# Kernel optimization log

Hardware: AMD Instinct MI355X
Metric: run time of the kernel (lower is better)

Reference implementation:

```python
import jax, jax.numpy as jnp
import numpy as np

B, S, D, H = 2, 2048, 1024, 16
HEAD_DIM = D // H
SCALE = HEAD_DIM ** -0.5


def setup_inputs() -> dict:
    key = jax.random.key(0)
    k1, k2, k3 = jax.random.split(key, 3)
    x = jax.random.normal(k1, (B, S, D), dtype=jnp.float32)
    # torch nn.Linear convention: weight is [out_features, in_features], y = x @ W.T + b
    W_qkv = jax.random.normal(k2, (3 * D, D), dtype=jnp.float32) * 0.02  # qkv Linear, bias=False
    W_out = jax.random.normal(k3, (D, D), dtype=jnp.float32) * 0.02
    b_out = jnp.zeros((D,), dtype=jnp.float32)
    return {"x": x, "W_qkv": W_qkv, "W_out": W_out, "b_out": b_out}


def reference(x, W_qkv, W_out, b_out):
    b, s, d_model = x.shape
    # qkv projection (no bias), then split 'b c (qkv h d) -> qkv b h c d'
    qkv = (x @ W_qkv.T).reshape(b, s, 3, H, HEAD_DIM).transpose(2, 0, 3, 1, 4)
    q, k, v = qkv[0], qkv[1], qkv[2]  # each [b, h, s, hd]
    # naive full attention: scores materialized as [b, h, s, s]
    attn = jax.nn.softmax(jnp.einsum('bhxd,bhyd->bhxy', q, k) * SCALE, axis=-1)
    # dropout is identity (rate 0 / eval mode)
    o = jnp.einsum('bhxy,bhyd->bhxd', attn, v)
    o = o.transpose(0, 2, 1, 3).reshape(b, s, d_model)  # 'b h c d -> b c (h d)'
    return o @ W_out.T + b_out
```

## Files before the change

kernel.cpp:

```cpp
#include <hip/hip_runtime.h>


typedef __attribute__((ext_vector_type(8))) short short8;
typedef __attribute__((ext_vector_type(4))) float f32x4;
typedef unsigned short ushort_t;
typedef unsigned int uint32;

#define AS1 __attribute__((address_space(1)))
#define AS3 __attribute__((address_space(3)))

__device__ __forceinline__ void gload_lds16(const void* gp, void* lp) {
    __builtin_amdgcn_global_load_lds((const AS1 void*)gp, (AS3 void*)lp, 16, 0, 0);
}

#if __has_builtin(__builtin_amdgcn_exp2f)
#define EXP2F(x) __builtin_amdgcn_exp2f(x)
#else
#define EXP2F(x) exp2f(x)
#endif

__device__ __forceinline__ uint32 rhu(float f) { return __float_as_uint(f) + 0x8000u; }
#if __has_builtin(__builtin_amdgcn_perm)
__device__ __forceinline__ uint32 pk2bf(float a, float b) {
    return __builtin_amdgcn_perm(rhu(b), rhu(a), 0x07060302u);
}
#else
__device__ __forceinline__ uint32 pk2bf(float a, float b) {
    return (rhu(a) >> 16) | (rhu(b) & 0xffff0000u);
}
#endif
__device__ __forceinline__ ushort_t f2bf(float f) { return (ushort_t)(rhu(f) >> 16); }

__global__ void cvt_all(const float* __restrict__ x, ushort_t* __restrict__ xb,
                        const float* __restrict__ wq, ushort_t* __restrict__ wqb,
                        const float* __restrict__ wo, ushort_t* __restrict__ wob) {
    int blk = blockIdx.x;
    const float* in; ushort_t* out;
    if (blk < 4096)      { in = x;  out = xb;  }
    else if (blk < 7168) { in = wq; out = wqb; blk -= 4096; }
    else                 { in = wo; out = wob; blk -= 7168; }
    const int i = (blk * 256 + threadIdx.x) * 4;
    const float4 v = *(const float4*)(in + i);
    uint2 pk;
    pk.x = pk2bf(v.x, v.y);
    pk.y = pk2bf(v.z, v.w);
    *(uint2*)(out + i) = pk;
}

__global__ __launch_bounds__(256, 2)
void gemm_qkv(const ushort_t* __restrict__ A, const ushort_t* __restrict__ B,
              ushort_t* __restrict__ Cb, ushort_t* __restrict__ vT,
              int M, int N, int K, int ldc, float qScale) {
    __shared__ ushort_t lA[2][128 * 32];
    __shared__ ushort_t lB[2][128 * 32];
    const int tid = threadIdx.x;
    const int wave = tid >> 6, lane = tid & 63;
    const int quad = lane >> 4, l16 = lane & 15;
    const int wr = wave >> 1, wc = wave & 1;
    const int mBase = blockIdx.y * 128, nBase = blockIdx.x * 128;

    f32x4 acc[4][4];
#pragma unroll
    for (int i = 0; i < 4; i++)
#pragma unroll
        for (int j = 0; j < 4; j++) acc[i][j] = (f32x4){0.f, 0.f, 0.f, 0.f};

    const int ar = tid >> 2;
    const int ac = (((tid & 3) ^ ((ar >> 1) & 3)) * 8);
    const int rsw = ((l16 >> 1) & 3);

    const ushort_t* aptr = A + (size_t)(mBase + ar) * K + ac;
    const ushort_t* bptr = B + (size_t)(nBase + ar) * K + ac;

#define G1_STAGE(buf, k0)                                                            \
    {                                                                                \
        _Pragma("unroll") for (int c = 0; c < 2; c++) {                              \
            gload_lds16(aptr + (size_t)(c * 64) * K + (k0), lA[buf] + c * 2048 + wave * 512); \
            gload_lds16(bptr + (size_t)(c * 64) * K + (k0), lB[buf] + c * 2048 + wave * 512); \
        }                                                                            \
    }

    G1_STAGE(0, 0);
    for (int k0 = 0; k0 < K; k0 += 32) {
        const int cur = (k0 >> 5) & 1;
        __syncthreads();
        if (k0 + 32 < K) G1_STAGE(cur ^ 1, k0 + 32);

        short8 af[4], bf[4];
#pragma unroll
        for (int i = 0; i < 4; i++)
            af[i] = *(const short8*)(lA[cur] + (wr * 64 + i * 16 + l16) * 32 + ((quad ^ rsw) * 8));
#pragma unroll
        for (int j = 0; j < 4; j++)
            bf[j] = *(const short8*)(lB[cur] + (wc * 64 + j * 16 + l16) * 32 + ((quad ^ rsw) * 8));
#pragma unroll
        for (int i = 0; i < 4; i++)
#pragma unroll
            for (int j = 0; j < 4; j++)
                acc[i][j] = __builtin_amdgcn_mfma_f32_16x16x32_bf16(af[i], bf[j], acc[i][j], 0, 0, 0);
    }

    if (nBase >= 2048) {
#pragma unroll
        for (int i = 0; i < 4; i++)
#pragma unroll
            for (int j = 0; j < 4; j++) {
                const int row0 = mBase + wr * 64 + i * 16 + quad * 4;
                const int col = nBase + wc * 64 + j * 16 + l16 - 2048;
                const int b = row0 >> 11, s0 = row0 & 2047;
                uint2 pk;
                pk.x = pk2bf(acc[i][j][0], acc[i][j][1]);
                pk.y = pk2bf(acc[i][j][2], acc[i][j][3]);
                *(uint2*)(vT + ((size_t)(b * 16) * 64 + col) * 2048 + s0) = pk;
            }
        return;
    }
    const float cs = (nBase < 1024) ? qScale : 1.0f;
#pragma unroll
    for (int i = 0; i < 4; i++)
#pragma unroll
        for (int j = 0; j < 4; j++)
#pragma unroll
            for (int r = 0; r < 4; r++) {
                const int row = mBase + wr * 64 + i * 16 + quad * 4 + r;
                const int col = nBase + wc * 64 + j * 16 + l16;
                Cb[(size_t)row * ldc + col] = f2bf(acc[i][j][r] * cs);
            }
}

__global__ __launch_bounds__(256, 2)
void gemm_out(const ushort_t* __restrict__ A, const ushort_t* __restrict__ B,
              float* __restrict__ Cf, const float* __restrict__ bias,
              int M, int N, int K) {
    __shared__ ushort_t lA[2][64 * 64];
    __shared__ ushort_t lB[2][128 * 64];
    const int tid = threadIdx.x;
    const int wave = tid >> 6, lane = tid & 63;
    const int quad = lane >> 4, l16 = lane & 15;
    const int mBase = blockIdx.y * 64, nBase = blockIdx.x * 128;

    f32x4 acc[4][2];
#pragma unroll
    for (int i = 0; i < 4; i++)
#pragma unroll
        for (int j = 0; j < 2; j++) acc[i][j] = (f32x4){0.f, 0.f, 0.f, 0.f};

    const int sr = tid >> 3;
    const int sc = ((tid & 7) ^ (sr & 7)) * 8;
    const int swz = l16 & 7;

    const ushort_t* aptr = A + (size_t)(mBase + sr) * K + sc;
    const ushort_t* bptr = B + (size_t)(nBase + sr) * K + sc;

#define G2_STAGE(buf, k0)                                                              \
    {                                                                                  \
        _Pragma("unroll") for (int c = 0; c < 2; c++)                                  \
            gload_lds16(aptr + (size_t)(c * 32) * K + (k0), lA[buf] + c * 2048 + wave * 512); \
        _Pragma("unroll") for (int c = 0; c < 4; c++)                                  \
            gload_lds16(bptr + (size_t)(c * 32) * K + (k0), lB[buf] + c * 2048 + wave * 512); \
    }

    G2_STAGE(0, 0);
    for (int k0 = 0; k0 < K; k0 += 64) {
        const int cur = (k0 >> 6) & 1;
        __syncthreads();
        if (k0 + 64 < K) G2_STAGE(cur ^ 1, k0 + 64);

#pragma unroll
        for (int ks = 0; ks < 2; ks++) {
            short8 af[4], bf[2];
#pragma unroll
            for (int i = 0; i < 4; i++)
                af[i] = *(const short8*)(lA[cur] + (i * 16 + l16) * 64 + (((ks * 4 + quad) ^ swz) * 8));
#pragma unroll
            for (int j = 0; j < 2; j++)
                bf[j] = *(const short8*)(lB[cur] + (wave * 32 + j * 16 + l16) * 64 + (((ks * 4 + quad) ^ swz) * 8));
#pragma unroll
            for (int i = 0; i < 4; i++)
#pragma unroll
                for (int j = 0; j < 2; j++)
                    acc[i][j] = __builtin_amdgcn_mfma_f32_16x16x32_bf16(af[i], bf[j], acc[i][j], 0, 0, 0);
        }
    }

#pragma unroll
    for (int i = 0; i < 4; i++)
#pragma unroll
        for (int j = 0; j < 2; j++)
#pragma unroll
            for (int r = 0; r < 4; r++) {
                const int row = mBase + i * 16 + quad * 4 + r;
                const int col = nBase + wave * 32 + j * 16 + l16;
                Cf[(size_t)row * N + col] = acc[i][j][r] + bias[col];
            }
}

__global__ __launch_bounds__(512, 4)
void attn_flash(const ushort_t* __restrict__ qk, const ushort_t* __restrict__ vT,
                ushort_t* __restrict__ o) {
    __shared__ ushort_t smem[26624];

    const int tid = threadIdx.x;
    const int wave = tid >> 6, lane = tid & 63;
    const int quad = lane >> 4, l16 = lane & 15;
    const int qg = wave & 3, kg = wave >> 2;
    const int bh = blockIdx.y, b = bh >> 4, h = bh & 15;
    const size_t rowBase = (size_t)b * 2048;
    const int qCol = h * 64, kCol = 1024 + h * 64;
    const int qRow0 = blockIdx.x * 128;
    const int swz = l16 & 7;

    ushort_t* lP = smem + 16384 + wave * 1280;

    {
        const int sr_ = tid >> 3;
        const int sc_ = ((tid & 7) ^ (sr_ & 7)) * 8;
#pragma unroll
        for (int cc = 0; cc < 2; cc++)
            gload_lds16(qk + (rowBase + qRow0 + cc * 64 + sr_) * 2048 + qCol + sc_,
                        smem + 16384 + cc * 4096 + wave * 512);
    }
    __syncthreads();
    short8 qf[2][2];
#pragma unroll
    for (int qt = 0; qt < 2; qt++)
#pragma unroll
        for (int ks = 0; ks < 2; ks++)
            qf[qt][ks] = *(const short8*)(smem + 16384 + (qg * 32 + qt * 16 + l16) * 64 +
                                          (((ks * 4 + quad) ^ swz) * 8));
    __syncthreads();

    short8 onesA;
#pragma unroll
    for (int i = 0; i < 8; i++) onesA[i] = (short)0x3F80;

    f32x4 oacc[4][2];
    f32x4 lacc[2];
#pragma unroll
    for (int qt = 0; qt < 2; qt++) {
        lacc[qt] = (f32x4){0.f, 0.f, 0.f, 0.f};
#pragma unroll
        for (int dt = 0; dt < 4; dt++) oacc[dt][qt] = (f32x4){0.f, 0.f, 0.f, 0.f};
    }

    const int sr = tid >> 3;
    const int sch = ((tid & 7) ^ (sr & 7)) * 8;
    const ushort_t* kptr = qk + (rowBase + sr) * 2048 + kCol + sch;
    const ushort_t* vptr = vT + ((size_t)bh * 64 + sr) * 2048 + sch;

#define AT_STAGE(buf, kt)                                                            \
    {                                                                                \
        gload_lds16(kptr + (size_t)(kt) * 64 * 2048, smem + (buf) * 4096 + wave * 512); \
        gload_lds16(vptr + (kt) * 64, smem + 8192 + (buf) * 4096 + wave * 512);      \
    }

    AT_STAGE(0, 0);
    for (int kt = 0; kt < 32; kt++) {
        const int cur = kt & 1;
        __syncthreads();
        if (kt < 31) AT_STAGE(cur ^ 1, kt + 1);
        const ushort_t* lK = smem + cur * 4096;
        const ushort_t* lV = smem + 8192 + cur * 4096;

        f32x4 sacc[2][2];
#pragma unroll
        for (int mh = 0; mh < 2; mh++) {
            const int krow = kg * 32 + mh * 16 + l16;
            const short8 k0 = *(const short8*)(lK + krow * 64 + ((quad ^ swz) * 8));
            const short8 k1 = *(const short8*)(lK + krow * 64 + (((4 + quad) ^ swz) * 8));
#pragma unroll
            for (int qt = 0; qt < 2; qt++) {
                f32x4 t = (f32x4){0.f, 0.f, 0.f, 0.f};
                t = __builtin_amdgcn_mfma_f32_16x16x32_bf16(k0, qf[qt][0], t, 0, 0, 0);
                t = __builtin_amdgcn_mfma_f32_16x16x32_bf16(k1, qf[qt][1], t, 0, 0, 0);
                sacc[mh][qt] = t;
            }
        }

#pragma unroll
        for (int qt = 0; qt < 2; qt++)
#pragma unroll
            for (int mh = 0; mh < 2; mh++) {
                const f32x4 s = sacc[mh][qt];
                uint2 pk;
                pk.x = pk2bf(EXP2F(s[0]), EXP2F(s[1]));
                pk.y = pk2bf(EXP2F(s[2]), EXP2F(s[3]));
                *(uint2*)(&lP[(qt * 16 + l16) * 40 + mh * 16 + quad * 4]) = pk;
            }

        short8 pf[2];
#pragma unroll
        for (int qt = 0; qt < 2; qt++) {
            pf[qt] = *(const short8*)(&lP[(qt * 16 + l16) * 40 + quad * 8]);
            lacc[qt] = __builtin_amdgcn_mfma_f32_16x16x32_bf16(onesA, pf[qt], lacc[qt], 0, 0, 0);
        }
#pragma unroll
        for (int dt = 0; dt < 4; dt++) {
            const short8 vf = *(const short8*)(lV + (dt * 16 + l16) * 64 +
                                               (((kg * 4 + quad) ^ swz) * 8));
#pragma unroll
            for (int qt = 0; qt < 2; qt++)
                oacc[dt][qt] = __builtin_amdgcn_mfma_f32_16x16x32_bf16(vf, pf[qt], oacc[dt][qt], 0, 0, 0);
        }
    }

    __syncthreads();
    float* red = (float*)smem;
    if (kg == 1) {
#pragma unroll
        for (int qt = 0; qt < 2; qt++) {
            if (quad == 0) red[8192 + qg * 32 + qt * 16 + l16] = lacc[qt][0];
#pragma unroll
            for (int dt = 0; dt < 4; dt++)
                *(f32x4*)(red + (((qg * 4 + dt) * 2 + qt) * 64 + lane) * 4) = oacc[dt][qt];
        }
    }
    __syncthreads();
    if (kg == 0) {
        float linv[2];
#pragma unroll
        for (int qt = 0; qt < 2; qt++)
            linv[qt] = 1.0f / (lacc[qt][0] + red[8192 + qg * 32 + qt * 16 + l16]);
#pragma unroll
        for (int qt = 0; qt < 2; qt++) {
            const size_t row = rowBase + qRow0 + qg * 32 + qt * 16 + l16;
#pragma unroll
            for (int dt = 0; dt < 4; dt++) {
                const f32x4 r = *(const f32x4*)(red + (((qg * 4 + dt) * 2 + qt) * 64 + lane) * 4);
                uint2 pk;
                pk.x = pk2bf((oacc[dt][qt][0] + r[0]) * linv[qt],
                             (oacc[dt][qt][1] + r[1]) * linv[qt]);
                pk.y = pk2bf((oacc[dt][qt][2] + r[2]) * linv[qt],
                             (oacc[dt][qt][3] + r[3]) * linv[qt]);
                *(uint2*)(o + row * 1024 + h * 64 + dt * 16 + quad * 4) = pk;
            }
        }
    }
}

extern "C" void kernel_launch(void* const* d_in, const int* in_sizes, int n_in,
                              void* d_out, int out_size, void* d_ws, size_t ws_size,
                              hipStream_t stream) {
    const float* x    = (const float*)d_in[0];
    const float* Wqkv = (const float*)d_in[1];
    const float* Wout = (const float*)d_in[2];
    const float* bout = (const float*)d_in[3];
    float* out = (float*)d_out;

    ushort_t* xb    = (ushort_t*)d_ws;
    ushort_t* wqkvb = xb + (size_t)4096 * 1024;
    ushort_t* woutb = wqkvb + (size_t)3072 * 1024;
    ushort_t* qkb   = woutb + (size_t)1024 * 1024;
    ushort_t* vTb   = qkb + (size_t)4096 * 2048;
    ushort_t* ob    = xb;

    const float SC = 0.125f * 1.44269504089f;

    cvt_all<<<8192, 256, 0, stream>>>(x, xb, Wqkv, wqkvb, Wout, woutb);
    gemm_qkv<<<dim3(24, 32), 256, 0, stream>>>(xb, wqkvb, qkb, vTb, 4096, 3072, 1024, 2048, SC);
    attn_flash<<<dim3(16, 32), 512, 0, stream>>>(qkb, vTb, ob);
    gemm_out<<<dim3(8, 64), 256, 0, stream>>>(ob, woutb, out, bout, 4096, 1024, 1024);
}
```

Measured before the change: 181.4 us.

## Fuse fp32-to-bf16 conversion into GEMM loads, drop separate convert kernel

Removes the standalone cvt_all kernel. The QKV and output-projection GEMMs now read fp32 inputs and weights directly into registers, pack them to bf16, and write them to shared memory after the MFMA loop, in place of asynchronous global-to-LDS loads. This avoids a kernel launch and a full round trip of bf16 copies through global memory. In exchange the GEMMs read twice the bytes, hold more registers for the staging buffers, and the qkv GEMM's launch bound rises to 3 blocks per CU.

Measured after the change: 186.0 us. 1.03x slower.

```diff
diff --git a/kernel.cpp b/kernel.cpp
--- a/kernel.cpp
+++ b/kernel.cpp
@@ -31,24 +31,15 @@
 #endif
 __device__ __forceinline__ ushort_t f2bf(float f) { return (ushort_t)(rhu(f) >> 16); }
 
-__global__ void cvt_all(const float* __restrict__ x, ushort_t* __restrict__ xb,
-                        const float* __restrict__ wq, ushort_t* __restrict__ wqb,
-                        const float* __restrict__ wo, ushort_t* __restrict__ wob) {
-    int blk = blockIdx.x;
-    const float* in; ushort_t* out;
-    if (blk < 4096)      { in = x;  out = xb;  }
-    else if (blk < 7168) { in = wq; out = wqb; blk -= 4096; }
-    else                 { in = wo; out = wob; blk -= 7168; }
-    const int i = (blk * 256 + threadIdx.x) * 4;
-    const float4 v = *(const float4*)(in + i);
-    uint2 pk;
-    pk.x = pk2bf(v.x, v.y);
-    pk.y = pk2bf(v.z, v.w);
-    *(uint2*)(out + i) = pk;
-}
-
-__global__ __launch_bounds__(256, 2)
-void gemm_qkv(const ushort_t* __restrict__ A, const ushort_t* __restrict__ B,
+__device__ __forceinline__ uint4 pk8bf(const float4 a, const float4 b) {
+    uint4 r;
+    r.x = pk2bf(a.x, a.y); r.y = pk2bf(a.z, a.w);
+    r.z = pk2bf(b.x, b.y); r.w = pk2bf(b.z, b.w);
+    return r;
+}
+
+__global__ __launch_bounds__(256, 3)
+void gemm_qkv(const float* __restrict__ A, const float* __restrict__ B,
               ushort_t* __restrict__ Cb, ushort_t* __restrict__ vT,
               int M, int N, int K, int ldc, float qScale) {
     __shared__ ushort_t lA[2][128 * 32];
@@ -66,25 +57,38 @@
         for (int j = 0; j < 4; j++) acc[i][j] = (f32x4){0.f, 0.f, 0.f, 0.f};
 
     const int ar = tid >> 2;
-    const int ac = (((tid & 3) ^ ((ar >> 1) & 3)) * 8);
+    const int scA = (((tid & 3) ^ ((ar >> 1) & 3)) * 8);
     const int rsw = ((l16 >> 1) & 3);
 
-    const ushort_t* aptr = A + (size_t)(mBase + ar) * K + ac;
-    const ushort_t* bptr = B + (size_t)(nBase + ar) * K + ac;
-
-#define G1_STAGE(buf, k0)                                                            \
-    {                                                                                \
-        _Pragma("unroll") for (int c = 0; c < 2; c++) {                              \
-            gload_lds16(aptr + (size_t)(c * 64) * K + (k0), lA[buf] + c * 2048 + wave * 512); \
-            gload_lds16(bptr + (size_t)(c * 64) * K + (k0), lB[buf] + c * 2048 + wave * 512); \
-        }                                                                            \
-    }
-
-    G1_STAGE(0, 0);
+    const float* aF = A + (size_t)(mBase + ar) * K + scA;
+    const float* bF = B + (size_t)(nBase + ar) * K + scA;
+
+    float4 ar0[2], ar1[2], br0[2], br1[2];
+
+#define G1_LOAD(k0)                                                        \
+    {                                                                      \
+        _Pragma("unroll") for (int c = 0; c < 2; c++) {                    \
+            ar0[c] = *(const float4*)(aF + (size_t)(c * 64) * K + (k0));   \
+            ar1[c] = *(const float4*)(aF + (size_t)(c * 64) * K + (k0) + 4); \
+            br0[c] = *(const float4*)(bF + (size_t)(c * 64) * K + (k0));   \
+            br1[c] = *(const float4*)(bF + (size_t)(c * 64) * K + (k0) + 4); \
+        }                                                                  \
+    }
+#define G1_WRITE(buf)                                                      \
+    {                                                                      \
+        _Pragma("unroll") for (int c = 0; c < 2; c++) {                    \
+            *(uint4*)(lA[buf] + c * 2048 + tid * 8) = pk8bf(ar0[c], ar1[c]); \
+            *(uint4*)(lB[buf] + c * 2048 + tid * 8) = pk8bf(br0[c], br1[c]); \
+        }                                                                  \
+    }
+
+    G1_LOAD(0);
+    G1_WRITE(0);
     for (int k0 = 0; k0 < K; k0 += 32) {
         const int cur = (k0 >> 5) & 1;
         __syncthreads();
-        if (k0 + 32 < K) G1_STAGE(cur ^ 1, k0 + 32);
+        const bool pf = (k0 + 32 < K);
+        if (pf) G1_LOAD(k0 + 32);
 
         short8 af[4], bf[4];
 #pragma unroll
@@ -98,6 +102,8 @@
 #pragma unroll
             for (int j = 0; j < 4; j++)
                 acc[i][j] = __builtin_amdgcn_mfma_f32_16x16x32_bf16(af[i], bf[j], acc[i][j], 0, 0, 0);
+
+        if (pf) G1_WRITE(cur ^ 1);
     }
 
     if (nBase >= 2048) {
@@ -129,7 +135,7 @@
 }
 
 __global__ __launch_bounds__(256, 2)
-void gemm_out(const ushort_t* __restrict__ A, const ushort_t* __restrict__ B,
+void gemm_out(const ushort_t* __restrict__ A, const float* __restrict__ B,
               float* __restrict__ Cf, const float* __restrict__ bias,
               int M, int N, int K) {
     __shared__ ushort_t lA[2][64 * 64];
@@ -150,21 +156,36 @@
     const int swz = l16 & 7;
 
     const ushort_t* aptr = A + (size_t)(mBase + sr) * K + sc;
-    const ushort_t* bptr = B + (size_t)(nBase + sr) * K + sc;
-
-#define G2_STAGE(buf, k0)                                                              \
-    {                                                                                  \
-        _Pragma("unroll") for (int c = 0; c < 2; c++)                                  \
+    const float* bF = B + (size_t)(nBase + sr) * K + sc;
+
+    float4 br0[4], br1[4];
+
+#define G2_ALOAD(buf, k0)                                                            \
+    {                                                                                \
+        _Pragma("unroll") for (int c = 0; c < 2; c++)                                \
             gload_lds16(aptr + (size_t)(c * 32) * K + (k0), lA[buf] + c * 2048 + wave * 512); \
-        _Pragma("unroll") for (int c = 0; c < 4; c++)                                  \
-            gload_lds16(bptr + (size_t)(c * 32) * K + (k0), lB[buf] + c * 2048 + wave * 512); \
-    }
-
-    G2_STAGE(0, 0);
+    }
+#define G2_BLOAD(k0)                                                                 \
+    {                                                                                \
+        _Pragma("unroll") for (int c = 0; c < 4; c++) {                              \
+            br0[c] = *(const float4*)(bF + (size_t)(c * 32) * K + (k0));             \
+            br1[c] = *(const float4*)(bF + (size_t)(c * 32) * K + (k0) + 4);         \
+        }                                                                            \
+    }
+#define G2_BWRITE(buf)                                                               \
+    {                                                                                \
+        _Pragma("unroll") for (int c = 0; c < 4; c++)                                \
+            *(uint4*)(lB[buf] + c * 2048 + tid * 8) = pk8bf(br0[c], br1[c]);         \
+    }
+
+    G2_BLOAD(0);
+    G2_ALOAD(0, 0);
+    G2_BWRITE(0);
     for (int k0 = 0; k0 < K; k0 += 64) {
         const int cur = (k0 >> 6) & 1;
         __syncthreads();
-        if (k0 + 64 < K) G2_STAGE(cur ^ 1, k0 + 64);
+        const bool pf = (k0 + 64 < K);
+        if (pf) { G2_BLOAD(k0 + 64); G2_ALOAD(cur ^ 1, k0 + 64); }
 
 #pragma unroll
         for (int ks = 0; ks < 2; ks++) {
@@ -181,6 +202,7 @@
                 for (int j = 0; j < 2; j++)
                     acc[i][j] = __builtin_amdgcn_mfma_f32_16x16x32_bf16(af[i], bf[j], acc[i][j], 0, 0, 0);
         }
+        if (pf) G2_BWRITE(cur ^ 1);
     }
 
 #pragma unroll
@@ -347,17 +369,13 @@
     const float* bout = (const float*)d_in[3];
     float* out = (float*)d_out;
 
-    ushort_t* xb    = (ushort_t*)d_ws;
-    ushort_t* wqkvb = xb + (size_t)4096 * 1024;
-    ushort_t* woutb = wqkvb + (size_t)3072 * 1024;
-    ushort_t* qkb   = woutb + (size_t)1024 * 1024;
-    ushort_t* vTb   = qkb + (size_t)4096 * 2048;
-    ushort_t* ob    = xb;
+    ushort_t* qkb = (ushort_t*)d_ws;
+    ushort_t* vTb = qkb + (size_t)4096 * 2048;
+    ushort_t* ob  = vTb + (size_t)32 * 64 * 2048;
 
     const float SC = 0.125f * 1.44269504089f;
 
-    cvt_all<<<8192, 256, 0, stream>>>(x, xb, Wqkv, wqkvb, Wout, woutb);
-    gemm_qkv<<<dim3(24, 32), 256, 0, stream>>>(xb, wqkvb, qkb, vTb, 4096, 3072, 1024, 2048, SC);
+    gemm_qkv<<<dim3(24, 32), 256, 0, stream>>>(x, Wqkv, qkb, vTb, 4096, 3072, 1024, 2048, SC);
     attn_flash<<<dim3(16, 32), 512, 0, stream>>>(qkb, vTb, ob);
-    gemm_out<<<dim3(8, 64), 256, 0, stream>>>(ob, woutb, out, bout, 4096, 1024, 1024);
-}
+    gemm_out<<<dim3(8, 64), 256, 0, stream>>>(ob, Wout, out, bout, 4096, 1024, 1024);
+}
```
